# Kernel optimization log

Hardware: AMD Instinct MI355X
Metric: run time of the kernel (lower is better)

Reference implementation:

```python
import jax, jax.numpy as jnp
import numpy as np
from jax import lax

NB = 8        # nbands
BS = 32       # block_size
MTF = 41      # MTF kernel size
N = BS * BS   # self.N = block_size**2


def _dwconv(x, k):
    # depthwise (groups=NB) VALID conv, NCHW / OIHW
    return lax.conv_general_dilated(
        x, k, window_strides=(1, 1), padding='VALID',
        dimension_numbers=('NCHW', 'OIHW', 'NCHW'),
        feature_group_count=NB)


def setup_inputs() -> dict:
    key = jax.random.key(0)
    k1, k2, k3 = jax.random.split(key, 3)
    outputs = jax.random.normal(k1, (4, NB, 552, 552), dtype=jnp.float32)
    labels = jax.random.normal(k2, (4, NB, 512, 512), dtype=jnp.float32)
    # frozen per-band MTF lowpass kernel (requires_grad=False in the original)
    mtf_kernel = jax.random.normal(k3, (NB, 1, MTF, MTF), dtype=jnp.float32) * 0.02
    return {"outputs": outputs, "labels": labels, "mtf_kernel": mtf_kernel}


def reference(outputs, labels, mtf_kernel):
    box = jnp.ones((NB, 1, BS, BS), dtype=jnp.float32)  # all-ones box kernel
    o = _dwconv(outputs, mtf_kernel)                    # [4,NB,512,512]
    # five box-sum (moving window sum) maps -> [4,NB,481,481]
    o_sum = _dwconv(o, box)
    l_sum = _dwconv(labels, box)
    o_sq_sum = _dwconv(o * o, box)
    l_sq_sum = _dwconv(labels * labels, box)
    ol_sum = _dwconv(o * labels, box)

    mul = o_sum * l_sum                     # outputs_labels_sum_mul
    sq = o_sum ** 2 + l_sum ** 2            # outputs_labels_sum_mul_sq
    numerator = 4.0 * (N * ol_sum - mul) * mul
    denom_temp = N * (o_sq_sum + l_sq_sum) - sq
    denominator = denom_temp * sq

    quality_map = jnp.ones_like(denominator)
    idx1 = (denom_temp == 0) & (sq != 0)
    quality_map = jnp.where(idx1, 2.0 * mul / jnp.where(idx1, sq, 1.0), quality_map)
    idx2 = denominator != 0
    quality_map = jnp.where(idx2, numerator / jnp.where(idx2, denominator, 1.0), quality_map)

    return 1.0 - jnp.mean(quality_map)
```

## Files before the change

kernel.cpp:

```cpp
#include <hip/hip_runtime.h>

#define NBANDS 8
#define BS 32
#define MTF 41
#define IMG 552
#define CONV 512
#define QOUT 481
#define NIMG 32
#define NN 1024.0f

#define TX 560
#define TY 576

typedef _Float16 half8 __attribute__((ext_vector_type(8)));
typedef float float4v __attribute__((ext_vector_type(4)));

__global__ __launch_bounds__(256) void prep_transpose(
    const float* __restrict__ in, _Float16* __restrict__ T)
{
    __shared__ _Float16 s[64][72];
    int bid = blockIdx.x;
    int img = bid / 81;
    int t = bid % 81;
    int ty = t / 9, tx2 = t % 9;
    int y0 = ty * 64, x0 = tx2 * 64;
    const float* ip = in + (size_t)img * IMG * IMG;

    for (int k = 0; k < 16; ++k) {
        int i = k * 256 + threadIdx.x;
        int r = i >> 6, c = i & 63;
        int y = y0 + r, x = x0 + c;
        float v = (y < IMG && x < IMG) ? ip[(size_t)y * IMG + x] : 0.f;
        s[c][r] = (_Float16)v;
    }
    __syncthreads();
    _Float16* Tp = T + (size_t)img * TX * TY;
    for (int k = 0; k < 2; ++k) {
        int i = k * 256 + threadIdx.x;
        int xi = i >> 3, g = i & 7;
        int x = x0 + xi;
        if (x < TX) {
            half8 v = *(const half8*)&s[xi][g * 8];
            *(half8*)&Tp[(size_t)x * TY + y0 + g * 8] = v;
        }
    }
}

__global__ __launch_bounds__(128) void prep_atab(
    const float* __restrict__ w, _Float16* __restrict__ A)
{
    int band = blockIdx.x / MTF;
    int kx = blockIdx.x % MTF;
    int s = threadIdx.x >> 6, lane = threadIdx.x & 63;
    int row = lane & 15;
    int kb = s * 32 + ((lane >> 4) << 3);
    const float* wp = w + band * MTF * MTF;
    half8 v;
#pragma unroll
    for (int j = 0; j < 8; ++j) {
        int ky = kb + j - row;
        v[j] = (ky >= 0 && ky < MTF) ? (_Float16)wp[ky * MTF + kx] : (_Float16)0.f;
    }
    *(half8*)&A[(((size_t)(band * MTF + kx) * 2 + s) << 9) + lane * 8] = v;
}

__global__ __launch_bounds__(256) void conv_mfma(
    const _Float16* __restrict__ T, const _Float16* __restrict__ Atab,
    float* __restrict__ out)
{
    __shared__ __align__(16) _Float16 sT[112 * 128];
    int bid = blockIdx.x;
    int img = bid >> 6;
    int t = bid & 63;
    int y0 = (t >> 3) << 6;
    int x0 = (t & 7) << 6;
    int band = img & 7;

    const _Float16* Tp = T + (size_t)img * TX * TY;
    {
        int g = threadIdx.x & 15;
        int xb = threadIdx.x >> 4;
        for (int it = 0; it < 7; ++it) {
            int x = xb + it * 16;
            half8 v = *(const half8*)&Tp[(size_t)(x0 + x) * TY + y0 + g * 8];
            int sw = x & 7;
            *(half8*)((char*)sT + ((x << 8) + ((g ^ sw) << 4))) = v;
        }
    }
    __syncthreads();

    int lane = threadIdx.x & 63;
    int wid  = threadIdx.x >> 6;
    int n = lane & 15, g4 = lane >> 4;
    int gyb = (wid << 1) + g4;
    const _Float16* Ap = Atab + (((size_t)band * MTF) << 10) + lane * 8;

    float4v acc[4];
#pragma unroll
    for (int i = 0; i < 4; ++i) acc[i] = (float4v){0.f, 0.f, 0.f, 0.f};

    for (int kx = 0; kx < MTF; ++kx) {
        half8 A0 = *(const half8*)(Ap);
        half8 A1 = *(const half8*)(Ap + 512);
        Ap += 1024;
        int xb0 = n + kx;
#pragma unroll
        for (int t2 = 0; t2 < 4; ++t2) {
            int x = xb0 + (t2 << 4);
            int sw = x & 7;
            half8 B0 = *(const half8*)((const char*)sT +
                        ((x << 8) + ((gyb ^ sw) << 4)));
            half8 B1 = *(const half8*)((const char*)sT +
                        ((x << 8) + (((gyb + 4) ^ sw) << 4)));
            acc[t2] = __builtin_amdgcn_mfma_f32_16x16x32_f16(A0, B0, acc[t2], 0, 0, 0);
            acc[t2] = __builtin_amdgcn_mfma_f32_16x16x32_f16(A1, B1, acc[t2], 0, 0, 0);
        }
    }

    float* op = out + (size_t)img * CONV * CONV;
    int row0 = y0 + (wid << 4) + (g4 << 2);
    int col0 = x0 + n;
#pragma unroll
    for (int t2 = 0; t2 < 4; ++t2) {
#pragma unroll
        for (int r = 0; r < 4; ++r)
            op[(size_t)(row0 + r) * CONV + col0 + (t2 << 4)] = acc[t2][r];
    }
}

#define H_STRIP 64

template<int C, int RM, int BM, bool BC>
__device__ __forceinline__ float dppadd(float v) {
    int t = __builtin_amdgcn_update_dpp(0, __builtin_bit_cast(int, v), C, RM, BM, BC);
    return v + __builtin_bit_cast(float, t);
}

__device__ __forceinline__ float wave_iscan(float v) {
    v = dppadd<0x111, 0xf, 0xf, true >(v);
    v = dppadd<0x112, 0xf, 0xf, true >(v);
    v = dppadd<0x114, 0xf, 0xf, true >(v);
    v = dppadd<0x118, 0xf, 0xf, true >(v);
    v = dppadd<0x142, 0xa, 0xf, false>(v);
    v = dppadd<0x143, 0xc, 0xf, false>(v);
    return v;
}

__device__ __forceinline__ float win32(float s, int lane) {
    float P = wave_iscan(s);
    float Pg = __shfl(P, lane + 31, 64);
    return Pg - P + s;
}

__global__ __launch_bounds__(512) void box_q_wave(
    const float* __restrict__ o,
    const float* __restrict__ lab,
    double* __restrict__ acc)
{
    int bid   = blockIdx.x;
    int img   = bid >> 4;
    int strip = (bid >> 1) & 7;
    int xblk  = bid & 1;
    int wid   = threadIdx.x >> 6;
    int lane  = threadIdx.x & 63;

    int c0 = xblk * 256 + wid * 32;
    int c  = c0 + lane;
    bool cvalid = c < CONV;
    int r0 = strip * H_STRIP;
    int nrows = min(H_STRIP, QOUT - r0);

    const float* op = o   + (size_t)img * CONV * CONV + c;
    const float* lp = lab + (size_t)img * CONV * CONV + c;

    float s0 = 0.f, s1 = 0.f, s2 = 0.f, s3 = 0.f, s4 = 0.f;
#pragma unroll 4
    for (int r = r0; r < r0 + BS; ++r) {
        float ov = cvalid ? op[(size_t)r * CONV] : 0.f;
        float lv = cvalid ? lp[(size_t)r * CONV] : 0.f;
        s0 += ov; s1 += lv; s2 += ov * ov; s3 += lv * lv; s4 += ov * lv;
    }

    int x = c0 + lane;
    bool xvalid = (lane < 32) && (x < QOUT);
    float qacc = 0.f;

    for (int i = 0;; ++i) {
        float oa = 0.f, la = 0.f, ob = 0.f, lb = 0.f;
        bool more = (i + 1 < nrows);
        if (more && cvalid) {
            int radd = r0 + i + BS, rsub = r0 + i;
            oa = op[(size_t)radd * CONV]; la = lp[(size_t)radd * CONV];
            ob = op[(size_t)rsub * CONV]; lb = lp[(size_t)rsub * CONV];
        }

        float A0 = win32(s0, lane);
        float A1 = win32(s1, lane);
        float A2 = win32(s2, lane);
        float A3 = win32(s3, lane);
        float A4 = win32(s4, lane);

        if (xvalid) {
            float mul = A0 * A1;
            float sq  = A0 * A0 + A1 * A1;
            float num = 4.f * (NN * A4 - mul) * mul;
            float dt  = NN * (A2 + A3) - sq;
            float den = dt * sq;
            float q = 1.f;
            if (dt == 0.f && sq != 0.f) q = 2.f * mul / sq;
            if (den != 0.f) q = num / den;
            qacc += q;
        }

        if (!more) break;
        s0 += oa - ob;
        s1 += la - lb;
        s2 += oa * oa - ob * ob;
        s3 += la * la - lb * lb;
        s4 += oa * la - ob * lb;
    }

    qacc += __shfl_down(qacc, 16, 64);
    qacc += __shfl_down(qacc, 8, 64);
    qacc += __shfl_down(qacc, 4, 64);
    qacc += __shfl_down(qacc, 2, 64);
    qacc += __shfl_down(qacc, 1, 64);
    if (lane == 0) atomicAdd(&acc[img], (double)qacc);
}

__global__ void finalize_kernel(const double* __restrict__ acc, float* __restrict__ out)
{
    double t = 0.0;
    for (int i = 0; i < NIMG; ++i) t += acc[i];
    out[0] = 1.0f - (float)(t / 7403552.0);
}

extern "C" void kernel_launch(void* const* d_in, const int* in_sizes, int n_in,
                              void* d_out, int out_size, void* d_ws, size_t ws_size,
                              hipStream_t stream)
{
    const float* outputs = (const float*)d_in[0];
    const float* labels  = (const float*)d_in[1];
    const float* mtf     = (const float*)d_in[2];

    double*    acc   = (double*)d_ws;
    float*     o_buf = (float*)((char*)d_ws + 4096);
    _Float16*  T     = (_Float16*)((char*)d_ws + 4096 + 33554432);
    _Float16*  Atab  = (_Float16*)((char*)d_ws + 4096 + 33554432 + 20643840);

    hipMemsetAsync(d_ws, 0, 256, stream);

    prep_transpose<<<NIMG * 81, 256, 0, stream>>>(outputs, T);
    prep_atab<<<NBANDS * MTF, 128, 0, stream>>>(mtf, Atab);
    conv_mfma<<<NIMG * 64, 256, 0, stream>>>(T, Atab, o_buf);
    box_q_wave<<<NIMG * 16, 512, 0, stream>>>(o_buf, labels, acc);
    finalize_kernel<<<1, 1, 0, stream>>>(acc, (float*)d_out);
}
```

Baseline: 139.3 us.

## Switch conv to 32x32x16 MFMA, merge box sums, halve strip height

The MTF convolution moves from 16x16x32 to 32x32x16 MFMA tiles. The filter table is rebuilt as five K-slices per column, and the LDS layout is changed to a padded, band-major one with two interleaved accumulators. The box-quality kernel merges the o² and l² sums into one scan, cutting the wave scans from five to four, and replaces the division with a fast reciprocal. It also halves the strip height to launch twice as many blocks. The reciprocal approximation and the merged sums slightly change numerics, and the shorter strips repeat the 32-row warm-up sum more often.

```diff
diff --git a/kernel.cpp b/kernel.cpp
--- a/kernel.cpp
+++ b/kernel.cpp
@@ -14,6 +14,7 @@
 
 typedef _Float16 half8 __attribute__((ext_vector_type(8)));
 typedef float float4v __attribute__((ext_vector_type(4)));
+typedef float f32x16 __attribute__((ext_vector_type(16)));
 
 __global__ __launch_bounds__(256) void prep_transpose(
     const float* __restrict__ in, _Float16* __restrict__ T)
@@ -46,29 +47,31 @@
     }
 }
 
-__global__ __launch_bounds__(128) void prep_atab(
+__global__ __launch_bounds__(320) void prep_atab32(
     const float* __restrict__ w, _Float16* __restrict__ A)
 {
-    int band = blockIdx.x / MTF;
-    int kx = blockIdx.x % MTF;
+    int bid = blockIdx.x;
+    int band = bid / MTF, kx = bid % MTF;
     int s = threadIdx.x >> 6, lane = threadIdx.x & 63;
-    int row = lane & 15;
-    int kb = s * 32 + ((lane >> 4) << 3);
+    int i = lane & 31;
+    int kb = 16 * s + ((lane >> 5) << 3);
     const float* wp = w + band * MTF * MTF;
     half8 v;
 #pragma unroll
     for (int j = 0; j < 8; ++j) {
-        int ky = kb + j - row;
+        int ky = kb + j - i;
         v[j] = (ky >= 0 && ky < MTF) ? (_Float16)wp[ky * MTF + kx] : (_Float16)0.f;
     }
-    *(half8*)&A[(((size_t)(band * MTF + kx) * 2 + s) << 9) + lane * 8] = v;
-}
-
-__global__ __launch_bounds__(256) void conv_mfma(
+    *(half8*)&A[(((size_t)bid * 5 + s) << 9) + lane * 8] = v;
+}
+
+#define XP 105
+
+__global__ __launch_bounds__(256) void conv_mfma32(
     const _Float16* __restrict__ T, const _Float16* __restrict__ Atab,
     float* __restrict__ out)
 {
-    __shared__ __align__(16) _Float16 sT[112 * 128];
+    __shared__ __align__(16) _Float16 sB[14 * XP * 8];
     int bid = blockIdx.x;
     int img = bid >> 6;
     int t = bid & 63;
@@ -78,57 +81,52 @@
 
     const _Float16* Tp = T + (size_t)img * TX * TY;
     {
-        int g = threadIdx.x & 15;
+        int g  = threadIdx.x & 15;
         int xb = threadIdx.x >> 4;
-        for (int it = 0; it < 7; ++it) {
-            int x = xb + it * 16;
-            half8 v = *(const half8*)&Tp[(size_t)(x0 + x) * TY + y0 + g * 8];
-            int sw = x & 7;
-            *(half8*)((char*)sT + ((x << 8) + ((g ^ sw) << 4))) = v;
+#pragma unroll
+        for (int p = 0; p < 7; ++p) {
+            int xx = xb + p * 16;
+            if (g < 14 && xx < 104) {
+                half8 v = *(const half8*)&Tp[(size_t)(x0 + xx) * TY + y0 + g * 8];
+                *(half8*)&sB[(g * XP + xx) * 8] = v;
+            }
         }
     }
     __syncthreads();
 
-    int lane = threadIdx.x & 63;
-    int wid  = threadIdx.x >> 6;
-    int n = lane & 15, g4 = lane >> 4;
-    int gyb = (wid << 1) + g4;
-    const _Float16* Ap = Atab + (((size_t)band * MTF) << 10) + lane * 8;
-
-    float4v acc[4];
-#pragma unroll
-    for (int i = 0; i < 4; ++i) acc[i] = (float4v){0.f, 0.f, 0.f, 0.f};
+    int l  = threadIdx.x & 63;
+    int w  = threadIdx.x >> 6;
+    int wy = w >> 1, wx = w & 1;
+    int xbase = wx * 32 + (l & 31);
+    int gb    = 4 * wy + (l >> 5);
+
+    const half8* Ap = (const half8*)(Atab + (((size_t)band * MTF * 5) << 9)) + l;
+
+    f32x16 acc0 = {}, acc1 = {};
 
     for (int kx = 0; kx < MTF; ++kx) {
-        half8 A0 = *(const half8*)(Ap);
-        half8 A1 = *(const half8*)(Ap + 512);
-        Ap += 1024;
-        int xb0 = n + kx;
-#pragma unroll
-        for (int t2 = 0; t2 < 4; ++t2) {
-            int x = xb0 + (t2 << 4);
-            int sw = x & 7;
-            half8 B0 = *(const half8*)((const char*)sT +
-                        ((x << 8) + ((gyb ^ sw) << 4)));
-            half8 B1 = *(const half8*)((const char*)sT +
-                        ((x << 8) + (((gyb + 4) ^ sw) << 4)));
-            acc[t2] = __builtin_amdgcn_mfma_f32_16x16x32_f16(A0, B0, acc[t2], 0, 0, 0);
-            acc[t2] = __builtin_amdgcn_mfma_f32_16x16x32_f16(A1, B1, acc[t2], 0, 0, 0);
-        }
-    }
+        const half8* Ak = Ap + (size_t)kx * 5 * 64;
+        int xk = xbase + kx;
+#pragma unroll
+        for (int s = 0; s < 5; ++s) {
+            half8 a = Ak[(size_t)s * 64];
+            half8 b = *(const half8*)&sB[((gb + 2 * s) * XP + xk) * 8];
+            if (s & 1) acc1 = __builtin_amdgcn_mfma_f32_32x32x16_f16(a, b, acc1, 0, 0, 0);
+            else       acc0 = __builtin_amdgcn_mfma_f32_32x32x16_f16(a, b, acc0, 0, 0, 0);
+        }
+    }
+#pragma unroll
+    for (int r = 0; r < 16; ++r) acc0[r] += acc1[r];
 
     float* op = out + (size_t)img * CONV * CONV;
-    int row0 = y0 + (wid << 4) + (g4 << 2);
-    int col0 = x0 + n;
-#pragma unroll
-    for (int t2 = 0; t2 < 4; ++t2) {
-#pragma unroll
-        for (int r = 0; r < 4; ++r)
-            op[(size_t)(row0 + r) * CONV + col0 + (t2 << 4)] = acc[t2][r];
-    }
-}
-
-#define H_STRIP 64
+    int col   = x0 + wx * 32 + (l & 31);
+    int rbase = y0 + wy * 32 + ((l >> 5) << 2);
+#pragma unroll
+    for (int r = 0; r < 16; ++r) {
+        int row = rbase + (r & 3) + ((r >> 2) << 3);
+        op[(size_t)row * CONV + col] = acc0[r];
+    }
+}
 
 template<int C, int RM, int BM, bool BC>
 __device__ __forceinline__ float dppadd(float v) {
@@ -152,14 +150,16 @@
     return Pg - P + s;
 }
 
+#define SROWS 31
+
 __global__ __launch_bounds__(512) void box_q_wave(
     const float* __restrict__ o,
     const float* __restrict__ lab,
     double* __restrict__ acc)
 {
     int bid   = blockIdx.x;
-    int img   = bid >> 4;
-    int strip = (bid >> 1) & 7;
+    int img   = bid >> 5;
+    int strip = (bid >> 1) & 15;
     int xblk  = bid & 1;
     int wid   = threadIdx.x >> 6;
     int lane  = threadIdx.x & 63;
@@ -167,18 +167,20 @@
     int c0 = xblk * 256 + wid * 32;
     int c  = c0 + lane;
     bool cvalid = c < CONV;
-    int r0 = strip * H_STRIP;
-    int nrows = min(H_STRIP, QOUT - r0);
+    int r0 = strip * SROWS;
+    int nrows = min(SROWS, QOUT - r0);
 
     const float* op = o   + (size_t)img * CONV * CONV + c;
     const float* lp = lab + (size_t)img * CONV * CONV + c;
 
-    float s0 = 0.f, s1 = 0.f, s2 = 0.f, s3 = 0.f, s4 = 0.f;
+    float s0 = 0.f, s1 = 0.f, s2 = 0.f, s3 = 0.f;
 #pragma unroll 4
     for (int r = r0; r < r0 + BS; ++r) {
         float ov = cvalid ? op[(size_t)r * CONV] : 0.f;
         float lv = cvalid ? lp[(size_t)r * CONV] : 0.f;
-        s0 += ov; s1 += lv; s2 += ov * ov; s3 += lv * lv; s4 += ov * lv;
+        s0 += ov; s1 += lv;
+        s2 = fmaf(ov, ov, fmaf(lv, lv, s2));
+        s3 = fmaf(ov, lv, s3);
     }
 
     int x = c0 + lane;
@@ -198,26 +200,24 @@
         float A1 = win32(s1, lane);
         float A2 = win32(s2, lane);
         float A3 = win32(s3, lane);
-        float A4 = win32(s4, lane);
 
         if (xvalid) {
             float mul = A0 * A1;
-            float sq  = A0 * A0 + A1 * A1;
-            float num = 4.f * (NN * A4 - mul) * mul;
-            float dt  = NN * (A2 + A3) - sq;
+            float sq  = fmaf(A0, A0, A1 * A1);
+            float num = 4.f * fmaf(NN, A3, -mul) * mul;
+            float dt  = fmaf(NN, A2, -sq);
             float den = dt * sq;
-            float q = 1.f;
-            if (dt == 0.f && sq != 0.f) q = 2.f * mul / sq;
-            if (den != 0.f) q = num / den;
-            qacc += q;
+            bool  c1  = (dt == 0.f) && (sq != 0.f);
+            float nn  = num, dd = den;
+            if (den == 0.f) { nn = c1 ? 2.f * mul : 1.f; dd = c1 ? sq : 1.f; }
+            qacc += nn * __builtin_amdgcn_rcpf(dd);
         }
 
         if (!more) break;
         s0 += oa - ob;
         s1 += la - lb;
-        s2 += oa * oa - ob * ob;
-        s3 += la * la - lb * lb;
-        s4 += oa * la - ob * lb;
+        s2 = fmaf(oa, oa, fmaf(la, la, fmaf(ob, -ob, fmaf(lb, -lb, s2))));
+        s3 = fmaf(oa, la, fmaf(ob, -lb, s3));
     }
 
     qacc += __shfl_down(qacc, 16, 64);
@@ -251,8 +251,8 @@
     hipMemsetAsync(d_ws, 0, 256, stream);
 
     prep_transpose<<<NIMG * 81, 256, 0, stream>>>(outputs, T);
-    prep_atab<<<NBANDS * MTF, 128, 0, stream>>>(mtf, Atab);
-    conv_mfma<<<NIMG * 64, 256, 0, stream>>>(T, Atab, o_buf);
-    box_q_wave<<<NIMG * 16, 512, 0, stream>>>(o_buf, labels, acc);
+    prep_atab32<<<NBANDS * MTF, 320, 0, stream>>>(mtf, Atab);
+    conv_mfma32<<<NIMG * 64, 256, 0, stream>>>(T, Atab, o_buf);
+    box_q_wave<<<NIMG * 32, 512, 0, stream>>>(o_buf, labels, acc);
     finalize_kernel<<<1, 1, 0, stream>>>(acc, (float*)d_out);
 }
```

Result: slower. 196.0 us (+40.8%).
